# Optimization experiments

Measured on AMD Instinct MI355X. Metric: run time of the kernel, lower is better.

Reference implementation:

```python
import jax, jax.numpy as jnp
import numpy as np

D_MODEL = 1024
NUM_HEADS = 16
HEAD_DIM = D_MODEL // NUM_HEADS  # 64
THETA = 10000.0
BATCH = 4
SEQ = 2048


def _rope(v, pos):
    # v: (n, h, s, d) with d even; pairs are interleaved: (..., d//2, 2)
    n, h, s, d = v.shape
    j = jnp.arange(d // 2, dtype=v.dtype)
    inv_freq = THETA ** (-2.0 * j / d)                     # (d/2,)
    angles = pos.astype(v.dtype)[:, None] * inv_freq[None, :]  # (s, d/2)
    c = jnp.cos(angles)[None, None]                        # (1,1,s,d/2)
    sn = jnp.sin(angles)[None, None]
    vb = v.reshape(n, h, s, d // 2, 2)
    x0, x1 = vb[..., 0], vb[..., 1]
    y0 = x0 * c - x1 * sn
    y1 = x0 * sn + x1 * c
    return jnp.stack([y0, y1], axis=-1).reshape(n, h, s, d)


def setup_inputs() -> dict:
    key = jax.random.key(0)
    ks = jax.random.split(key, 5)
    x = jax.random.normal(ks[0], (BATCH, SEQ, D_MODEL), dtype=jnp.float32)
    token_positions = jnp.arange(SEQ, dtype=jnp.int32)
    scale = 0.02  # keep activations in a numerically sane range
    W_Q = jax.random.normal(ks[1], (D_MODEL, D_MODEL), dtype=jnp.float32) * scale
    W_K = jax.random.normal(ks[2], (D_MODEL, D_MODEL), dtype=jnp.float32) * scale
    W_V = jax.random.normal(ks[3], (D_MODEL, D_MODEL), dtype=jnp.float32) * scale
    W_O = jax.random.normal(ks[4], (D_MODEL, D_MODEL), dtype=jnp.float32) * scale
    return {"x": x, "token_positions": token_positions,
            "W_Q": W_Q, "W_K": W_K, "W_V": W_V, "W_O": W_O}


def reference(x, token_positions, W_Q, W_K, W_V, W_O):
    n, s, _ = x.shape
    h, d = NUM_HEADS, HEAD_DIM
    # projections: Linear stores W as (out, in), applies x @ W.T
    Q = (x @ W_Q.T).reshape(n, s, h, d).transpose(0, 2, 1, 3)  # (n,h,s,d)
    K = (x @ W_K.T).reshape(n, s, h, d).transpose(0, 2, 1, 3)
    V = (x @ W_V.T).reshape(n, s, h, d).transpose(0, 2, 1, 3)
    Q = _rope(Q, token_positions)
    K = _rope(K, token_positions)
    scores = jnp.einsum('nhqd,nhkd->nhqk', Q, K) * (d ** -0.5)
    causal = jnp.tril(jnp.ones((s, s), dtype=bool))
    scores = jnp.where(causal[None, None], scores, -jnp.inf)
    attn = jax.nn.softmax(scores, axis=-1)
    out = jnp.einsum('nhqk,nhkd->nhqd', attn, V)
    out = out.transpose(0, 2, 1, 3).reshape(n, s, h * d)
    return out @ W_O.T
```

## Files before the change

### kernel.cpp

```cpp
#include <hip/hip_runtime.h>
#include <math.h>

#define DM 1024
#define NH 16
#define HD 64
#define SQ 2048
#define NB 4
#define MR (NB*SQ)
#define TTOT ((size_t)MR * DM)

typedef unsigned short ushort_t;
typedef __attribute__((ext_vector_type(8)))  short bf16x8;
typedef __attribute__((ext_vector_type(4)))  float f32x4;
typedef __attribute__((ext_vector_type(16))) float f32x16;

__device__ __forceinline__ ushort_t f2bf(float f) {
    unsigned u = __float_as_uint(f);
    return (ushort_t)((u + 0x7fffu + ((u >> 16) & 1u)) >> 16);
}
__device__ __forceinline__ float bf2f(ushort_t u) {
    return __uint_as_float((unsigned)u << 16);
}

__device__ __forceinline__ void gload16(const void* g, void* l) {
    __builtin_amdgcn_global_load_lds(
        (const __attribute__((address_space(1))) void*)g,
        (__attribute__((address_space(3))) void*)l, 16, 0, 0);
}

__device__ __forceinline__ unsigned cvtpk_bf16(float a, float b) {
    unsigned r;
    asm volatile("v_cvt_pk_bf16_f32 %0, %1, %2" : "=v"(r) : "v"(a), "v"(b));
    return r;
}

__global__ __launch_bounds__(256)
void f2bf_kernel(const float* __restrict__ in, ushort_t* __restrict__ out) {
    int i = (blockIdx.x * 256 + threadIdx.x) * 4;
    float4 v = *reinterpret_cast<const float4*>(&in[i]);
    ushort4 o;
    o.x = f2bf(v.x); o.y = f2bf(v.y); o.z = f2bf(v.z); o.w = f2bf(v.w);
    *reinterpret_cast<ushort4*>(&out[i]) = o;
}

__global__ __launch_bounds__(256)
void w4_convert(const float* __restrict__ w0, const float* __restrict__ w1,
                const float* __restrict__ w2, const float* __restrict__ w3,
                ushort_t* __restrict__ out) {
    int i = (blockIdx.x * 256 + threadIdx.x) * 4;
    const int WSZ = DM * DM;
    const float* src = (i < WSZ) ? w0 : (i < 2 * WSZ) ? w1
                     : (i < 3 * WSZ) ? w2 : w3;
    int off = i & (WSZ - 1);
    float4 v = *reinterpret_cast<const float4*>(&src[off]);
    ushort4 o;
    o.x = f2bf(v.x); o.y = f2bf(v.y); o.z = f2bf(v.z); o.w = f2bf(v.w);
    *reinterpret_cast<ushort4*>(&out[i]) = o;
}

template<int MODE>
__global__ __launch_bounds__(256)
void gemm_bf16_bt(const ushort_t* __restrict__ A, const ushort_t* __restrict__ B,
                  void* __restrict__ Cv, int M, int N, int K, float scale)
{
    __shared__ ushort_t As[128 * 32];
    __shared__ ushort_t Bs[128 * 32];

    const int tid = threadIdx.x;
    const int w  = tid >> 6;
    const int l  = tid & 63;
    const int wr = w >> 1, wc = w & 1;
    const int arow0 = blockIdx.y * 128;
    const int bcol0 = blockIdx.x * 128;
    const int lr = l & 15;
    const int kg = l >> 4;

    const int srow[2] = { (w * 2 + 0) * 16 + (l >> 2), (w * 2 + 1) * 16 + (l >> 2) };
    const int scol = (l & 3) * 8;

    f32x4 acc[4][4] = {};

    for (int k0 = 0; k0 < K; k0 += 32) {
        #pragma unroll
        for (int q = 0; q < 2; ++q) {
            int chunk = w * 2 + q;
            gload16(&A[(size_t)(arow0 + srow[q]) * K + k0 + scol], &As[chunk * 512]);
            gload16(&B[(size_t)(bcol0 + srow[q]) * K + k0 + scol], &Bs[chunk * 512]);
        }
        __syncthreads();

        bf16x8 af[4], bfr[4];
        #pragma unroll
        for (int m = 0; m < 4; ++m)
            af[m] = *reinterpret_cast<const bf16x8*>(
                        &As[(wr * 64 + m * 16 + lr) * 32 + kg * 8]);
        #pragma unroll
        for (int nn = 0; nn < 4; ++nn)
            bfr[nn] = *reinterpret_cast<const bf16x8*>(
                        &Bs[(wc * 64 + nn * 16 + lr) * 32 + kg * 8]);

        #pragma unroll
        for (int m = 0; m < 4; ++m)
            #pragma unroll
            for (int nn = 0; nn < 4; ++nn)
                acc[m][nn] = __builtin_amdgcn_mfma_f32_16x16x32_bf16(
                    af[m], bfr[nn], acc[m][nn], 0, 0, 0);
        __syncthreads();
    }

    const int crow = kg * 4;
    #pragma unroll
    for (int m = 0; m < 4; ++m) {
        #pragma unroll
        for (int nn = 0; nn < 4; ++nn) {
            #pragma unroll
            for (int r = 0; r < 4; ++r) {
                int row = arow0 + wr * 64 + m * 16 + crow + r;
                int col = bcol0 + wc * 64 + nn * 16 + lr;
                float v = acc[m][nn][r] * scale;
                if (MODE == 0) {
                    ((float*)Cv)[(size_t)row * N + col] = v;
                } else if (MODE == 2) {
                    int hh = row >> 6,  d = row & 63;
                    int nb = col >> 11, s = col & (SQ - 1);
                    ((ushort_t*)Cv)[(((size_t)nb * NH + hh) * HD + d) * SQ + s] = f2bf(v);
                } else {
                    int nb = row >> 11, s = row & (SQ - 1);
                    bool isq = (col < 1024);
                    int cc = col & 1023;
                    int hh = cc >> 6, d = cc & 63;
                    size_t idx = (((size_t)nb * NH + hh) * SQ + s) * HD + d;
                    float vv = isq ? v * 0.125f : v;
                    ((ushort_t*)Cv)[(isq ? (size_t)0 : TTOT) + idx] = f2bf(vv);
                }
            }
        }
    }
}

__global__ __launch_bounds__(256)
void rope_bf16(ushort_t* __restrict__ Q, ushort_t* __restrict__ K,
               const int* __restrict__ pos)
{
    int t = blockIdx.x * 256 + threadIdx.x;
    int j  = t & 31;
    int s  = (t >> 5) & (SQ - 1);
    int nh = t >> 16;
    size_t base = ((size_t)nh * SQ + s) * HD + 2 * j;

    float p = (float)pos[s];
    float inv = exp2f(-0.41524101186072848f * (float)j);
    float sn, cs;
    sincosf(p * inv, &sn, &cs);

    ushort2 q2 = *reinterpret_cast<ushort2*>(&Q[base]);
    ushort2 k2 = *reinterpret_cast<ushort2*>(&K[base]);
    float qx = bf2f(q2.x), qy = bf2f(q2.y);
    float kx = bf2f(k2.x), ky = bf2f(k2.y);
    ushort2 qo, ko;
    qo.x = f2bf(qx * cs - qy * sn);  qo.y = f2bf(qx * sn + qy * cs);
    ko.x = f2bf(kx * cs - ky * sn);  ko.y = f2bf(kx * sn + ky * cs);
    *reinterpret_cast<ushort2*>(&Q[base]) = qo;
    *reinterpret_cast<ushort2*>(&K[base]) = ko;
}

__global__ __launch_bounds__(256)
void flash_mfma(const ushort_t* __restrict__ Q, const ushort_t* __restrict__ K,
                const ushort_t* __restrict__ Vt, ushort_t* __restrict__ O)
{
    __shared__ ushort_t Ks [2][64 * 64];
    __shared__ ushort_t Vts[2][64 * 64];

    const int tid  = threadIdx.x;
    const int wq   = tid >> 6;
    const int lane = tid & 63;
    const int q5   = lane & 31;
    const int g    = lane >> 5;
    const int qb   = (gridDim.x - 1) - blockIdx.x;
    const int h    = blockIdx.y;
    const int n    = blockIdx.z;

    const size_t hb = (size_t)(n * NH + h);
    const ushort_t* Kp  = K  + hb * SQ * HD;
    const ushort_t* Vtp = Vt + hb * HD * SQ;

    const int qglob = qb * 128 + wq * 32 + q5;
    const int qwave = qb * 128 + wq * 32;
    const int qmaxw = qwave + 31;
    const int nt    = 2 * qb + 2;

    bf16x8 qf[4];
    {
        const ushort_t* Qr = Q + (hb * SQ + (size_t)qglob) * HD;
        #pragma unroll
        for (int s4 = 0; s4 < 4; ++s4)
            qf[s4] = *reinterpret_cast<const bf16x8*>(&Qr[s4 * 16 + g * 8]);
    }

    const int srowl = (lane >> 3);
    const int scole = ((lane & 7) ^ srowl) * 8;

    auto stage = [&](int buf, int t) {
        const int kvb = t * 64;
        #pragma unroll
        for (int qi = 0; qi < 2; ++qi) {
            int c = wq * 2 + qi;
            int row = c * 8 + srowl;
            gload16(&Kp [(size_t)(kvb + row) * HD + scole], &Ks [buf][c * 512]);
            gload16(&Vtp[(size_t)row * SQ + kvb + scole],   &Vts[buf][c * 512]);
        }
    };

    f32x16 o0 = {}, o1 = {};
    float m_run = -1e30f, l_run = 0.f;

    stage(0, 0);
    __syncthreads();

    for (int t = 0; t < nt; ++t) {
        const int cur = t & 1;
        const int kvbase = t * 64;

        if (t + 1 < nt) stage(cur ^ 1, t + 1);

        if (kvbase <= qmaxw) {
            f32x16 st0 = {}, st1 = {};
            #pragma unroll
            for (int s4 = 0; s4 < 4; ++s4) {
                {   int row = q5;
                    int c16 = (s4 * 2 + g) ^ (row & 7);
                    bf16x8 kf = *reinterpret_cast<const bf16x8*>(&Ks[cur][row * 64 + c16 * 8]);
                    st0 = __builtin_amdgcn_mfma_f32_32x32x16_bf16(kf, qf[s4], st0, 0, 0, 0);
                }
                {   int row = 32 + q5;
                    int c16 = (s4 * 2 + g) ^ (row & 7);
                    bf16x8 kf = *reinterpret_cast<const bf16x8*>(&Ks[cur][row * 64 + c16 * 8]);
                    st1 = __builtin_amdgcn_mfma_f32_32x32x16_bf16(kf, qf[s4], st1, 0, 0, 0);
                }
            }

            if (kvbase + 63 > qwave) {
                #pragma unroll
                for (int r = 0; r < 16; ++r) {
                    int kvr = kvbase + (r & 3) + 8 * (r >> 2) + 4 * g;
                    if (kvr      > qglob) st0[r] = -1e30f;
                    if (kvr + 32 > qglob) st1[r] = -1e30f;
                }
            }

            float pmax = -1e30f;
            #pragma unroll
            for (int r = 0; r < 16; ++r) {
                pmax = fmaxf(pmax, st0[r]);
                pmax = fmaxf(pmax, st1[r]);
            }
            pmax = fmaxf(pmax, __shfl_xor(pmax, 32));

            if (!__all(pmax - m_run <= 8.0f)) {
                float mnew = fmaxf(m_run, pmax);
                float sc = __expf(m_run - mnew);
                l_run *= sc;
                #pragma unroll
                for (int r = 0; r < 16; ++r) {
                    float scb = __shfl(sc, (r & 3) + 8 * (r >> 2) + 4 * g, 64);
                    o0[r] *= scb;
                    o1[r] *= scb;
                }
                m_run = mnew;
            }

            float rs = 0.f;
            #pragma unroll
            for (int r = 0; r < 16; ++r) {
                st0[r] = __expf(st0[r] - m_run); rs += st0[r];
                st1[r] = __expf(st1[r] - m_run); rs += st1[r];
            }
            rs += __shfl_xor(rs, 32);
            l_run += rs;

            #pragma unroll
            for (int s = 0; s < 4; ++s) {
                const int bA = (s & 1) * 8;
                const int bB = bA + 4;
                float pa0, pa1, pa2, pa3, pb0, pb1, pb2, pb3;
                if (s < 2) {
                    pa0 = st0[bA]; pa1 = st0[bA+1]; pa2 = st0[bA+2]; pa3 = st0[bA+3];
                    pb0 = st0[bB]; pb1 = st0[bB+1]; pb2 = st0[bB+2]; pb3 = st0[bB+3];
                } else {
                    pa0 = st1[bA]; pa1 = st1[bA+1]; pa2 = st1[bA+2]; pa3 = st1[bA+3];
                    pb0 = st1[bB]; pb1 = st1[bB+1]; pb2 = st1[bB+2]; pb3 = st1[bB+3];
                }
                unsigned wA0 = cvtpk_bf16(pa0, pa1), wA1 = cvtpk_bf16(pa2, pa3);
                unsigned wB0 = cvtpk_bf16(pb0, pb1), wB1 = cvtpk_bf16(pb2, pb3);

                unsigned send0 = g ? wA0 : wB0;
                unsigned send1 = g ? wA1 : wB1;
                unsigned recv0 = (unsigned)__shfl_xor((int)send0, 32, 64);
                unsigned recv1 = (unsigned)__shfl_xor((int)send1, 32, 64);

                unsigned d0 = g ? recv0 : wA0;
                unsigned d1 = g ? recv1 : wA1;
                unsigned d2 = g ? wB0 : recv0;
                unsigned d3 = g ? wB1 : recv1;

                int4 pi = make_int4((int)d0, (int)d1, (int)d2, (int)d3);
                bf16x8 pa = *reinterpret_cast<bf16x8*>(&pi);

                {   int row = q5;
                    int c16 = (s * 2 + g) ^ (row & 7);
                    bf16x8 vf = *reinterpret_cast<const bf16x8*>(&Vts[cur][row * 64 + c16 * 8]);
                    o0 = __builtin_amdgcn_mfma_f32_32x32x16_bf16(pa, vf, o0, 0, 0, 0);
                }
                {   int row = 32 + q5;
                    int c16 = (s * 2 + g) ^ (row & 7);
                    bf16x8 vf = *reinterpret_cast<const bf16x8*>(&Vts[cur][row * 64 + c16 * 8]);
                    o1 = __builtin_amdgcn_mfma_f32_32x32x16_bf16(pa, vf, o1, 0, 0, 0);
                }
            }
        }

        __syncthreads();
    }

    float linv = 1.0f / l_run;
    #pragma unroll
    for (int r = 0; r < 16; ++r) {
        int qr = (r & 3) + 8 * (r >> 2) + 4 * g;
        float lb = __shfl(linv, qr, 64);
        size_t rowb = ((size_t)n * SQ + qb * 128 + wq * 32 + qr) * DM + h * 64;
        O[rowb + q5]      = f2bf(o0[r] * lb);
        O[rowb + 32 + q5] = f2bf(o1[r] * lb);
    }
}

extern "C" void kernel_launch(void* const* d_in, const int* in_sizes, int n_in,
                              void* d_out, int out_size, void* d_ws, size_t ws_size,
                              hipStream_t stream)
{
    const float* x   = (const float*)d_in[0];
    const int*   pos = (const int*)  d_in[1];
    const float* W_Q = (const float*)d_in[2];
    const float* W_K = (const float*)d_in[3];
    const float* W_V = (const float*)d_in[4];
    const float* W_O = (const float*)d_in[5];
    float* out = (float*)d_out;

    const size_t T   = TTOT;
    const size_t WSZ = (size_t)DM * DM;

    ushort_t* xb  = (ushort_t*)d_ws;
    ushort_t* Wb  = xb + T;
    ushort_t* Qb  = Wb + 4 * WSZ;
    ushort_t* Kb  = Qb + T;
    ushort_t* Vtb = Kb + T;
    ushort_t* Op  = xb;

    const ushort_t* WVb = Wb + 2 * WSZ;
    const ushort_t* WOb = Wb + 3 * WSZ;

    f2bf_kernel<<<T / 1024, 256, 0, stream>>>(x, xb);
    w4_convert<<<4 * WSZ / 1024, 256, 0, stream>>>(W_Q, W_K, W_V, W_O, Wb);

    dim3 gQK(2048 / 128, MR / 128);
    gemm_bf16_bt<3><<<gQK, 256, 0, stream>>>(xb, Wb, Qb, MR, 2048, DM, 1.0f);
    dim3 gV(MR / 128, DM / 128);
    gemm_bf16_bt<2><<<gV, 256, 0, stream>>>(WVb, xb, Vtb, DM, MR, DM, 1.0f);

    rope_bf16<<<(NB * NH * SQ * 32) / 256, 256, 0, stream>>>(Qb, Kb, pos);

    dim3 agrid(SQ / 128, NH, NB);
    flash_mfma<<<agrid, 256, 0, stream>>>(Qb, Kb, Vtb, Op);

    dim3 gO(DM / 128, MR / 128);
    gemm_bf16_bt<0><<<gO, 256, 0, stream>>>(Op, WOb, out, MR, DM, DM, 1.0f);
}
```

Measured before the change: 354.4 us.

## Split attention KV range across waves with LDS merge; swizzle GEMM block order

The flash attention kernel now gives each block only 32 query rows. Its four waves split the KV tiles between them, loading K and V fragments straight from global memory instead of staging them through shared memory. Each wave's partial max, sum and output are then merged through LDS at the end. This makes the grid four times larger and avoids block-wide barriers in the loop, but K and V are now read redundantly per wave from cache rather than shared once. Separately, the GEMM kernel remaps block indices in an interleaved order by eight, presumably to spread neighbouring tiles across XCDs for cache locality.

New measurement: 425.8 us. +20.1%, slower.

```diff
diff --git a/kernel.cpp b/kernel.cpp
--- a/kernel.cpp
+++ b/kernel.cpp
@@ -70,8 +70,15 @@
     const int w  = tid >> 6;
     const int l  = tid & 63;
     const int wr = w >> 1, wc = w & 1;
-    const int arow0 = blockIdx.y * 128;
-    const int bcol0 = blockIdx.x * 128;
+
+    const int lin  = blockIdx.y * gridDim.x + blockIdx.x;
+    const int nwg8 = (gridDim.x * gridDim.y) >> 3;
+    const int nl   = (lin & 7) * nwg8 + (lin >> 3);
+    const int bx   = nl % gridDim.x;
+    const int by   = nl / gridDim.x;
+
+    const int arow0 = by * 128;
+    const int bcol0 = bx * 128;
     const int lr = l & 15;
     const int kg = l >> 4;
 
@@ -168,15 +175,15 @@
 void flash_mfma(const ushort_t* __restrict__ Q, const ushort_t* __restrict__ K,
                 const ushort_t* __restrict__ Vt, ushort_t* __restrict__ O)
 {
-    __shared__ ushort_t Ks [2][64 * 64];
-    __shared__ ushort_t Vts[2][64 * 64];
+    __shared__ float Op[4][64][33];
+    __shared__ float Ml[4][2][32];
 
     const int tid  = threadIdx.x;
-    const int wq   = tid >> 6;
+    const int wv   = tid >> 6;
     const int lane = tid & 63;
     const int q5   = lane & 31;
     const int g    = lane >> 5;
-    const int qb   = (gridDim.x - 1) - blockIdx.x;
+    const int qq   = (gridDim.x - 1) - blockIdx.x;
     const int h    = blockIdx.y;
     const int n    = blockIdx.z;
 
@@ -184,10 +191,8 @@
     const ushort_t* Kp  = K  + hb * SQ * HD;
     const ushort_t* Vtp = Vt + hb * HD * SQ;
 
-    const int qglob = qb * 128 + wq * 32 + q5;
-    const int qwave = qb * 128 + wq * 32;
-    const int qmaxw = qwave + 31;
-    const int nt    = 2 * qb + 2;
+    const int qglob = qq * 32 + q5;
+    const int nt    = (qq >> 1) + 1;
 
     bf16x8 qf[4];
     {
@@ -197,139 +202,141 @@
             qf[s4] = *reinterpret_cast<const bf16x8*>(&Qr[s4 * 16 + g * 8]);
     }
 
-    const int srowl = (lane >> 3);
-    const int scole = ((lane & 7) ^ srowl) * 8;
-
-    auto stage = [&](int buf, int t) {
-        const int kvb = t * 64;
-        #pragma unroll
-        for (int qi = 0; qi < 2; ++qi) {
-            int c = wq * 2 + qi;
-            int row = c * 8 + srowl;
-            gload16(&Kp [(size_t)(kvb + row) * HD + scole], &Ks [buf][c * 512]);
-            gload16(&Vtp[(size_t)row * SQ + kvb + scole],   &Vts[buf][c * 512]);
-        }
-    };
-
     f32x16 o0 = {}, o1 = {};
     float m_run = -1e30f, l_run = 0.f;
 
-    stage(0, 0);
-    __syncthreads();
-
-    for (int t = 0; t < nt; ++t) {
-        const int cur = t & 1;
+    for (int t = wv; t < nt; t += 4) {
         const int kvbase = t * 64;
 
-        if (t + 1 < nt) stage(cur ^ 1, t + 1);
-
-        if (kvbase <= qmaxw) {
-            f32x16 st0 = {}, st1 = {};
-            #pragma unroll
-            for (int s4 = 0; s4 < 4; ++s4) {
-                {   int row = q5;
-                    int c16 = (s4 * 2 + g) ^ (row & 7);
-                    bf16x8 kf = *reinterpret_cast<const bf16x8*>(&Ks[cur][row * 64 + c16 * 8]);
-                    st0 = __builtin_amdgcn_mfma_f32_32x32x16_bf16(kf, qf[s4], st0, 0, 0, 0);
-                }
-                {   int row = 32 + q5;
-                    int c16 = (s4 * 2 + g) ^ (row & 7);
-                    bf16x8 kf = *reinterpret_cast<const bf16x8*>(&Ks[cur][row * 64 + c16 * 8]);
-                    st1 = __builtin_amdgcn_mfma_f32_32x32x16_bf16(kf, qf[s4], st1, 0, 0, 0);
-                }
-            }
-
-            if (kvbase + 63 > qwave) {
-                #pragma unroll
-                for (int r = 0; r < 16; ++r) {
-                    int kvr = kvbase + (r & 3) + 8 * (r >> 2) + 4 * g;
-                    if (kvr      > qglob) st0[r] = -1e30f;
-                    if (kvr + 32 > qglob) st1[r] = -1e30f;
-                }
-            }
-
-            float pmax = -1e30f;
+        bf16x8 kf0[4], kf1[4];
+        #pragma unroll
+        for (int s4 = 0; s4 < 4; ++s4)
+            kf0[s4] = *reinterpret_cast<const bf16x8*>(
+                &Kp[(size_t)(kvbase + q5) * HD + s4 * 16 + g * 8]);
+        #pragma unroll
+        for (int s4 = 0; s4 < 4; ++s4)
+            kf1[s4] = *reinterpret_cast<const bf16x8*>(
+                &Kp[(size_t)(kvbase + 32 + q5) * HD + s4 * 16 + g * 8]);
+        bf16x8 vf0[4], vf1[4];
+        #pragma unroll
+        for (int s = 0; s < 4; ++s)
+            vf0[s] = *reinterpret_cast<const bf16x8*>(
+                &Vtp[(size_t)q5 * SQ + kvbase + s * 16 + g * 8]);
+        #pragma unroll
+        for (int s = 0; s < 4; ++s)
+            vf1[s] = *reinterpret_cast<const bf16x8*>(
+                &Vtp[(size_t)(32 + q5) * SQ + kvbase + s * 16 + g * 8]);
+
+        f32x16 st0 = {}, st1 = {};
+        #pragma unroll
+        for (int s4 = 0; s4 < 4; ++s4) {
+            st0 = __builtin_amdgcn_mfma_f32_32x32x16_bf16(kf0[s4], qf[s4], st0, 0, 0, 0);
+            st1 = __builtin_amdgcn_mfma_f32_32x32x16_bf16(kf1[s4], qf[s4], st1, 0, 0, 0);
+        }
+
+        if (kvbase + 63 > qq * 32) {
             #pragma unroll
             for (int r = 0; r < 16; ++r) {
-                pmax = fmaxf(pmax, st0[r]);
-                pmax = fmaxf(pmax, st1[r]);
+                int kvr = kvbase + (r & 3) + 8 * (r >> 2) + 4 * g;
+                if (kvr      > qglob) st0[r] = -1e30f;
+                if (kvr + 32 > qglob) st1[r] = -1e30f;
             }
-            pmax = fmaxf(pmax, __shfl_xor(pmax, 32));
-
-            if (!__all(pmax - m_run <= 8.0f)) {
-                float mnew = fmaxf(m_run, pmax);
-                float sc = __expf(m_run - mnew);
-                l_run *= sc;
-                #pragma unroll
-                for (int r = 0; r < 16; ++r) {
-                    float scb = __shfl(sc, (r & 3) + 8 * (r >> 2) + 4 * g, 64);
-                    o0[r] *= scb;
-                    o1[r] *= scb;
-                }
-                m_run = mnew;
-            }
-
-            float rs = 0.f;
+        }
+
+        float pmax = -1e30f;
+        #pragma unroll
+        for (int r = 0; r < 16; ++r) {
+            pmax = fmaxf(pmax, st0[r]);
+            pmax = fmaxf(pmax, st1[r]);
+        }
+        pmax = fmaxf(pmax, __shfl_xor(pmax, 32));
+
+        if (!__all(pmax - m_run <= 8.0f)) {
+            float mnew = fmaxf(m_run, pmax);
+            float sc = __expf(m_run - mnew);
+            l_run *= sc;
             #pragma unroll
             for (int r = 0; r < 16; ++r) {
-                st0[r] = __expf(st0[r] - m_run); rs += st0[r];
-                st1[r] = __expf(st1[r] - m_run); rs += st1[r];
+                float scb = __shfl(sc, (r & 3) + 8 * (r >> 2) + 4 * g, 64);
+                o0[r] *= scb;
+                o1[r] *= scb;
             }
-            rs += __shfl_xor(rs, 32);
-            l_run += rs;
-
-            #pragma unroll
-            for (int s = 0; s < 4; ++s) {
-                const int bA = (s & 1) * 8;
-                const int bB = bA + 4;
-                float pa0, pa1, pa2, pa3, pb0, pb1, pb2, pb3;
-                if (s < 2) {
-                    pa0 = st0[bA]; pa1 = st0[bA+1]; pa2 = st0[bA+2]; pa3 = st0[bA+3];
-                    pb0 = st0[bB]; pb1 = st0[bB+1]; pb2 = st0[bB+2]; pb3 = st0[bB+3];
-                } else {
-                    pa0 = st1[bA]; pa1 = st1[bA+1]; pa2 = st1[bA+2]; pa3 = st1[bA+3];
-                    pb0 = st1[bB]; pb1 = st1[bB+1]; pb2 = st1[bB+2]; pb3 = st1[bB+3];
-                }
-                unsigned wA0 = cvtpk_bf16(pa0, pa1), wA1 = cvtpk_bf16(pa2, pa3);
-                unsigned wB0 = cvtpk_bf16(pb0, pb1), wB1 = cvtpk_bf16(pb2, pb3);
-
-                unsigned send0 = g ? wA0 : wB0;
-                unsigned send1 = g ? wA1 : wB1;
-                unsigned recv0 = (unsigned)__shfl_xor((int)send0, 32, 64);
-                unsigned recv1 = (unsigned)__shfl_xor((int)send1, 32, 64);
-
-                unsigned d0 = g ? recv0 : wA0;
-                unsigned d1 = g ? recv1 : wA1;
-                unsigned d2 = g ? wB0 : recv0;
-                unsigned d3 = g ? wB1 : recv1;
-
-                int4 pi = make_int4((int)d0, (int)d1, (int)d2, (int)d3);
-                bf16x8 pa = *reinterpret_cast<bf16x8*>(&pi);
-
-                {   int row = q5;
-                    int c16 = (s * 2 + g) ^ (row & 7);
-                    bf16x8 vf = *reinterpret_cast<const bf16x8*>(&Vts[cur][row * 64 + c16 * 8]);
-                    o0 = __builtin_amdgcn_mfma_f32_32x32x16_bf16(pa, vf, o0, 0, 0, 0);
-                }
-                {   int row = 32 + q5;
-                    int c16 = (s * 2 + g) ^ (row & 7);
-                    bf16x8 vf = *reinterpret_cast<const bf16x8*>(&Vts[cur][row * 64 + c16 * 8]);
-                    o1 = __builtin_amdgcn_mfma_f32_32x32x16_bf16(pa, vf, o1, 0, 0, 0);
-                }
+            m_run = mnew;
+        }
+
+        float rs = 0.f;
+        #pragma unroll
+        for (int r = 0; r < 16; ++r) {
+            st0[r] = __expf(st0[r] - m_run); rs += st0[r];
+            st1[r] = __expf(st1[r] - m_run); rs += st1[r];
+        }
+        rs += __shfl_xor(rs, 32);
+        l_run += rs;
+
+        #pragma unroll
+        for (int s = 0; s < 4; ++s) {
+            const int bA = (s & 1) * 8;
+            const int bB = bA + 4;
+            float pa0, pa1, pa2, pa3, pb0, pb1, pb2, pb3;
+            if (s < 2) {
+                pa0 = st0[bA]; pa1 = st0[bA+1]; pa2 = st0[bA+2]; pa3 = st0[bA+3];
+                pb0 = st0[bB]; pb1 = st0[bB+1]; pb2 = st0[bB+2]; pb3 = st0[bB+3];
+            } else {
+                pa0 = st1[bA]; pa1 = st1[bA+1]; pa2 = st1[bA+2]; pa3 = st1[bA+3];
+                pb0 = st1[bB]; pb1 = st1[bB+1]; pb2 = st1[bB+2]; pb3 = st1[bB+3];
             }
-        }
-
-        __syncthreads();
-    }
-
-    float linv = 1.0f / l_run;
+            unsigned wA0 = cvtpk_bf16(pa0, pa1), wA1 = cvtpk_bf16(pa2, pa3);
+            unsigned wB0 = cvtpk_bf16(pb0, pb1), wB1 = cvtpk_bf16(pb2, pb3);
+
+            unsigned send0 = g ? wA0 : wB0;
+            unsigned send1 = g ? wA1 : wB1;
+            unsigned recv0 = (unsigned)__shfl_xor((int)send0, 32, 64);
+            unsigned recv1 = (unsigned)__shfl_xor((int)send1, 32, 64);
+
+            unsigned d0 = g ? recv0 : wA0;
+            unsigned d1 = g ? recv1 : wA1;
+            unsigned d2 = g ? wB0 : recv0;
+            unsigned d3 = g ? wB1 : recv1;
+
+            int4 pi = make_int4((int)d0, (int)d1, (int)d2, (int)d3);
+            bf16x8 pa = *reinterpret_cast<bf16x8*>(&pi);
+
+            o0 = __builtin_amdgcn_mfma_f32_32x32x16_bf16(pa, vf0[s], o0, 0, 0, 0);
+            o1 = __builtin_amdgcn_mfma_f32_32x32x16_bf16(pa, vf1[s], o1, 0, 0, 0);
+        }
+    }
+
+    if (g == 0) {
+        Ml[wv][0][q5] = m_run;
+        Ml[wv][1][q5] = l_run;
+    }
     #pragma unroll
     for (int r = 0; r < 16; ++r) {
-        int qr = (r & 3) + 8 * (r >> 2) + 4 * g;
-        float lb = __shfl(linv, qr, 64);
-        size_t rowb = ((size_t)n * SQ + qb * 128 + wq * 32 + qr) * DM + h * 64;
-        O[rowb + q5]      = f2bf(o0[r] * lb);
-        O[rowb + 32 + q5] = f2bf(o1[r] * lb);
+        Op[wv][lane][r]      = o0[r];
+        Op[wv][lane][16 + r] = o1[r];
+    }
+    __syncthreads();
+
+    if (wv == 0) {
+        #pragma unroll
+        for (int r = 0; r < 16; ++r) {
+            int qr = (r & 3) + 8 * (r >> 2) + 4 * g;
+            float m0 = Ml[0][0][qr], m1 = Ml[1][0][qr];
+            float m2 = Ml[2][0][qr], m3 = Ml[3][0][qr];
+            float mx = fmaxf(fmaxf(m0, m1), fmaxf(m2, m3));
+            float f0 = __expf(m0 - mx), f1 = __expf(m1 - mx);
+            float f2 = __expf(m2 - mx), f3 = __expf(m3 - mx);
+            float lsum = Ml[0][1][qr] * f0 + Ml[1][1][qr] * f1
+                       + Ml[2][1][qr] * f2 + Ml[3][1][qr] * f3;
+            float inv = 1.0f / lsum;
+            float v0 = (o0[r] * f0 + Op[1][lane][r]      * f1
+                      + Op[2][lane][r]      * f2 + Op[3][lane][r]      * f3) * inv;
+            float v1 = (o1[r] * f0 + Op[1][lane][16 + r] * f1
+                      + Op[2][lane][16 + r] * f2 + Op[3][lane][16 + r] * f3) * inv;
+            size_t rowb = ((size_t)n * SQ + qq * 32 + qr) * DM + h * 64;
+            O[rowb + q5]      = f2bf(v0);
+            O[rowb + 32 + q5] = f2bf(v1);
+        }
     }
 }
 
@@ -368,7 +375,7 @@
 
     rope_bf16<<<(NB * NH * SQ * 32) / 256, 256, 0, stream>>>(Qb, Kb, pos);
 
-    dim3 agrid(SQ / 128, NH, NB);
+    dim3 agrid(SQ / 32, NH, NB);
     flash_mfma<<<agrid, 256, 0, stream>>>(Qb, Kb, Vtb, Op);
 
     dim3 gO(DM / 128, MR / 128);
```
